# Performance work log

Hardware: AMD Instinct MI355X
Metric: run time of the kernel (lower is better)

Reference implementation:

```python
import jax, jax.numpy as jnp
import numpy as np

NUM_HEADS = 12
HEAD_DIM = 64
SCALE = HEAD_DIM ** -0.5


def setup_inputs() -> dict:
    key = jax.random.key(0)
    ks = jax.random.split(key, 5)
    B, N, C = 8, 1024, 768
    x = jax.random.normal(ks[0], (B, N, C), dtype=jnp.float32)
    qkv_w = jax.random.normal(ks[1], (3 * C, C), dtype=jnp.float32) * (C ** -0.5)
    qkv_b = jax.random.normal(ks[2], (3 * C,), dtype=jnp.float32) * 0.02
    proj_w = jax.random.normal(ks[3], (C, C), dtype=jnp.float32) * (C ** -0.5)
    proj_b = jax.random.normal(ks[4], (C,), dtype=jnp.float32) * 0.02
    return {"x": x, "qkv_w": qkv_w, "qkv_b": qkv_b, "proj_w": proj_w, "proj_b": proj_b}


def reference(x, qkv_w, qkv_b, proj_w, proj_b):
    B, N, C = x.shape
    H, D = NUM_HEADS, HEAD_DIM
    # qkv projection: (B,N,3C) -> (3,B,H,N,D)
    qkv = (x @ qkv_w.T + qkv_b).reshape(B, N, 3, H, D).transpose(2, 0, 3, 1, 4)
    q, k, v = qkv[0], qkv[1], qkv[2]
    q = q * SCALE
    # full N x N attention scores, softmax over keys
    attn = jax.nn.softmax(jnp.einsum("bhnd,bhmd->bhnm", q, k), axis=-1)
    # Libragrad: detach the softmax map before multiplying with V
    attn = jax.lax.stop_gradient(attn)
    out = jnp.einsum("bhnm,bhmd->bhnd", attn, v)  # (B,H,N,D)
    out = out.transpose(0, 2, 1, 3).reshape(B, N, C)
    return out @ proj_w.T + proj_b
```

## Files before the change

kernel.cpp:

```cpp
#include <hip/hip_runtime.h>

#define NH 12
#define HD 64
#define BB 8
#define SEQ 1024
#define CD 768

typedef __bf16 bf16x8 __attribute__((ext_vector_type(8)));
typedef float f32x4 __attribute__((ext_vector_type(4)));

__device__ __forceinline__ unsigned short f2bf(float f) {
    unsigned int u = __float_as_uint(f);
    u = (u + 0x7fffu + ((u >> 16) & 1u)) >> 16;
    return (unsigned short)u;
}

__device__ __forceinline__ void gld_lds16(const unsigned short* g, unsigned short* l) {
    __builtin_amdgcn_global_load_lds(
        (const __attribute__((address_space(1))) unsigned int*)g,
        (__attribute__((address_space(3))) unsigned int*)l, 16, 0, 0);
}

#define N4_X 1572864
#define N4_W1 442368
#define N4_W2 147456
__global__ void cast_all(const float* __restrict__ x, const float* __restrict__ w1,
                         const float* __restrict__ w2,
                         unsigned short* __restrict__ ox, unsigned short* __restrict__ ow1,
                         unsigned short* __restrict__ ow2) {
    int i = blockIdx.x * blockDim.x + threadIdx.x;
    const float4* src;
    ushort4* dst;
    if (i < N4_X) {
        src = (const float4*)x + i; dst = (ushort4*)ox + i;
    } else if (i < N4_X + N4_W1) {
        src = (const float4*)w1 + (i - N4_X); dst = (ushort4*)ow1 + (i - N4_X);
    } else if (i < N4_X + N4_W1 + N4_W2) {
        src = (const float4*)w2 + (i - N4_X - N4_W1); dst = (ushort4*)ow2 + (i - N4_X - N4_W1);
    } else return;
    float4 f = *src;
    ushort4 o;
    o.x = f2bf(f.x); o.y = f2bf(f.y); o.z = f2bf(f.z); o.w = f2bf(f.w);
    *dst = o;
}

template<int MODE>
__global__ __launch_bounds__(256)
void gemm_bt(const unsigned short* __restrict__ A, const unsigned short* __restrict__ W,
             const float* __restrict__ bias,
             unsigned short* __restrict__ qb, unsigned short* __restrict__ kb,
             unsigned short* __restrict__ vb, float* __restrict__ fout,
             int M, int N, int K) {
    __shared__ __attribute__((aligned(16))) unsigned short As[128 * 32];
    __shared__ __attribute__((aligned(16))) unsigned short Bs[128 * 32];

    const int t    = threadIdx.x;
    const int bm0  = blockIdx.x * 128;
    const int bn0  = blockIdx.y * 128;
    const int wave = t >> 6;
    const int lane = t & 63;
    const int wm   = (wave >> 1) * 64;
    const int wn   = (wave & 1) * 64;
    const int col  = lane & 15;
    const int quad = lane >> 4;

    const int srow = t >> 2;
    const int scol = (t & 3) * 8;

    f32x4 acc[4][4];
#pragma unroll
    for (int i = 0; i < 4; i++)
#pragma unroll
        for (int j = 0; j < 4; j++) acc[i][j] = (f32x4){0.f, 0.f, 0.f, 0.f};

    for (int k0 = 0; k0 < K; k0 += 32) {
        __syncthreads();
        gld_lds16(A + (size_t)(bm0 + srow) * K + k0 + scol,      As + srow * 32 + scol);
        gld_lds16(A + (size_t)(bm0 + 64 + srow) * K + k0 + scol, As + (64 + srow) * 32 + scol);
        gld_lds16(W + (size_t)(bn0 + srow) * K + k0 + scol,      Bs + srow * 32 + scol);
        gld_lds16(W + (size_t)(bn0 + 64 + srow) * K + k0 + scol, Bs + (64 + srow) * 32 + scol);
        __syncthreads();

        bf16x8 af[4], bf[4];
#pragma unroll
        for (int mi = 0; mi < 4; mi++)
            af[mi] = *(const bf16x8*)(As + (wm + mi * 16 + col) * 32 + quad * 8);
#pragma unroll
        for (int ni = 0; ni < 4; ni++)
            bf[ni] = *(const bf16x8*)(Bs + (wn + ni * 16 + col) * 32 + quad * 8);
#pragma unroll
        for (int mi = 0; mi < 4; mi++)
#pragma unroll
            for (int ni = 0; ni < 4; ni++)
                acc[mi][ni] = __builtin_amdgcn_mfma_f32_16x16x32_bf16(
                    af[mi], bf[ni], acc[mi][ni], 0, 0, 0);
    }

    if (MODE == 1) {
#pragma unroll
        for (int mi = 0; mi < 4; mi++)
#pragma unroll
            for (int ni = 0; ni < 4; ni++) {
                const int n = bn0 + wn + ni * 16 + col;
                const float bv = bias[n];
#pragma unroll
                for (int r = 0; r < 4; r++) {
                    const int m = bm0 + wm + mi * 16 + quad * 4 + r;
                    fout[(size_t)m * N + n] = acc[mi][ni][r] + bv;
                }
            }
        return;
    }

    const int sel = bn0 / 768;
    const int nb  = bn0 - sel * 768;
    const int b   = bm0 >> 10;
    const int nqb = bm0 & 1023;

    if (sel == 2) {
#pragma unroll
        for (int ni = 0; ni < 4; ni++) {
            const int hn = nb + wn + ni * 16;
            const int h  = hn >> 6;
            const int d0 = hn & 63;
            const float bv = bias[bn0 + wn + ni * 16 + col];
            unsigned short* const rowb =
                vb + ((size_t)(b * NH + h) * HD + d0 + col) * SEQ + nqb + wm;
#pragma unroll
            for (int mi = 0; mi < 4; mi++) {
                ushort4 o;
                o.x = f2bf(acc[mi][ni][0] + bv);
                o.y = f2bf(acc[mi][ni][1] + bv);
                o.z = f2bf(acc[mi][ni][2] + bv);
                o.w = f2bf(acc[mi][ni][3] + bv);
                *(ushort4*)(rowb + mi * 16 + quad * 4) = o;
            }
        }
        return;
    }

    unsigned short* const dstbuf = (sel == 0) ? qb : kb;
    const float scale = (sel == 0) ? 0.18033688f : 1.0f;

#pragma unroll
    for (int ni = 0; ni < 4; ni++) {
        const int hn = nb + wn + ni * 16;
        const int h  = hn >> 6;
        const int d0 = hn & 63;
        const float bv = bias[bn0 + wn + ni * 16 + col];
        unsigned short* const rowbase =
            dstbuf + ((size_t)(b * NH + h) * SEQ) * HD + d0 + col;
#pragma unroll
        for (int mi = 0; mi < 4; mi++)
#pragma unroll
            for (int r = 0; r < 4; r++) {
                const int nq = nqb + wm + mi * 16 + quad * 4 + r;
                rowbase[(size_t)nq * HD] = f2bf((acc[mi][ni][r] + bv) * scale);
            }
    }
}

__global__ __launch_bounds__(256, 3)
void attn_mfma(const unsigned short* __restrict__ qb,
               const unsigned short* __restrict__ kb,
               const unsigned short* __restrict__ vb,
               unsigned short* __restrict__ ob) {
    __shared__ __attribute__((aligned(16))) unsigned short Ks[64 * 72];
    __shared__ __attribute__((aligned(16))) unsigned short VT[64 * 72];
    __shared__ __attribute__((aligned(16))) unsigned short Ps[128 * 76];

    const int t  = threadIdx.x;
    const int bh = blockIdx.x;
    const int qt = blockIdx.y;
    const size_t base = (size_t)bh * SEQ * HD;

    const int sr = t >> 2;
    const int sc = (t & 3) * 16;

    const int wave = t >> 6;
    const int lane = t & 63;
    const int col  = lane & 15;
    const int quad = lane >> 4;

    bf16x8 aq[2][2];
#pragma unroll
    for (int u = 0; u < 2; u++) {
        const int q = qt * 128 + (2 * wave + u) * 16 + col;
        aq[u][0] = *(const bf16x8*)(qb + base + (size_t)q * HD + quad * 8);
        aq[u][1] = *(const bf16x8*)(qb + base + (size_t)q * HD + 32 + quad * 8);
    }

    float l_r[2] = {0.f, 0.f};
    f32x4 accO[2][4];
#pragma unroll
    for (int u = 0; u < 2; u++)
#pragma unroll
        for (int di = 0; di < 4; di++) accO[u][di] = (f32x4){0.f, 0.f, 0.f, 0.f};

    const unsigned short* kp = kb + base + (size_t)sr * HD + sc;
    const unsigned short* vp = vb + base + (size_t)sr * SEQ + sc;
    uint4 kr0 = *(const uint4*)kp,  kr1 = *(const uint4*)(kp + 8);
    uint4 vr0 = *(const uint4*)vp,  vr1 = *(const uint4*)(vp + 8);

    for (int kc = 0; kc < 16; kc++) {
        __syncthreads();
        *(uint4*)(Ks + sr * 72 + sc)     = kr0;
        *(uint4*)(Ks + sr * 72 + sc + 8) = kr1;
        *(uint4*)(VT + sr * 72 + sc)     = vr0;
        *(uint4*)(VT + sr * 72 + sc + 8) = vr1;
        __syncthreads();

        if (kc < 15) {
            const unsigned short* kn = kp + (size_t)(kc + 1) * 64 * HD;
            const unsigned short* vn = vp + (size_t)(kc + 1) * 64;
            kr0 = *(const uint4*)kn; kr1 = *(const uint4*)(kn + 8);
            vr0 = *(const uint4*)vn; vr1 = *(const uint4*)(vn + 8);
        }

        f32x4 accT[2][4];
#pragma unroll
        for (int ni = 0; ni < 4; ni++) {
            bf16x8 bk0 = *(const bf16x8*)(Ks + (ni * 16 + col) * 72 + quad * 8);
            bf16x8 bk1 = *(const bf16x8*)(Ks + (ni * 16 + col) * 72 + 32 + quad * 8);
#pragma unroll
            for (int u = 0; u < 2; u++) {
                f32x4 z = (f32x4){0.f, 0.f, 0.f, 0.f};
                z = __builtin_amdgcn_mfma_f32_16x16x32_bf16(bk0, aq[u][0], z, 0, 0, 0);
                z = __builtin_amdgcn_mfma_f32_16x16x32_bf16(bk1, aq[u][1], z, 0, 0, 0);
                accT[u][ni] = z;
            }
        }

#pragma unroll
        for (int u = 0; u < 2; u++) {
            const int prow = (2 * wave + u) * 16;
#pragma unroll
            for (int ni = 0; ni < 4; ni++) {
                float p0 = __builtin_exp2f(accT[u][ni][0]);
                float p1 = __builtin_exp2f(accT[u][ni][1]);
                float p2 = __builtin_exp2f(accT[u][ni][2]);
                float p3 = __builtin_exp2f(accT[u][ni][3]);
                l_r[u] += (p0 + p1) + (p2 + p3);
                union { __bf16 b[4]; uint2 u2; } pk;
                pk.b[0] = (__bf16)p0; pk.b[1] = (__bf16)p1;
                pk.b[2] = (__bf16)p2; pk.b[3] = (__bf16)p3;
                *(uint2*)(Ps + (prow + col) * 76 + ni * 16 + quad * 4) = pk.u2;
            }
        }

        bf16x8 ap[2][2];
#pragma unroll
        for (int u = 0; u < 2; u++) {
            const int prow = (2 * wave + u) * 16;
            ap[u][0] = *(const bf16x8*)(Ps + (prow + col) * 76 + quad * 8);
            ap[u][1] = *(const bf16x8*)(Ps + (prow + col) * 76 + 32 + quad * 8);
        }
#pragma unroll
        for (int di = 0; di < 4; di++) {
            bf16x8 bv0 = *(const bf16x8*)(VT + (di * 16 + col) * 72 + quad * 8);
            bf16x8 bv1 = *(const bf16x8*)(VT + (di * 16 + col) * 72 + 32 + quad * 8);
#pragma unroll
            for (int u = 0; u < 2; u++) {
                accO[u][di] = __builtin_amdgcn_mfma_f32_16x16x32_bf16(ap[u][0], bv0, accO[u][di], 0, 0, 0);
                accO[u][di] = __builtin_amdgcn_mfma_f32_16x16x32_bf16(ap[u][1], bv1, accO[u][di], 0, 0, 0);
            }
        }
    }

    const int b = bh / NH, h = bh - b * NH;
#pragma unroll
    for (int u = 0; u < 2; u++) {
        float s = l_r[u];
        s += __shfl_xor(s, 16);
        s += __shfl_xor(s, 32);
#pragma unroll
        for (int r = 0; r < 4; r++) {
            const float inv = 1.f / __shfl(s, quad * 4 + r);
            const int q = qt * 128 + (2 * wave + u) * 16 + quad * 4 + r;
            const size_t rowbase = ((size_t)b * SEQ + q) * CD + h * 64;
#pragma unroll
            for (int di = 0; di < 4; di++)
                ob[rowbase + di * 16 + col] = f2bf(accO[u][di][r] * inv);
        }
    }
}

extern "C" void kernel_launch(void* const* d_in, const int* in_sizes, int n_in,
                              void* d_out, int out_size, void* d_ws, size_t ws_size,
                              hipStream_t stream) {
    const float* x      = (const float*)d_in[0];
    const float* qkv_w  = (const float*)d_in[1];
    const float* qkv_b  = (const float*)d_in[2];
    const float* proj_w = (const float*)d_in[3];
    const float* proj_b = (const float*)d_in[4];
    float* out = (float*)d_out;

    char* ws = (char*)d_ws;
    unsigned short* x_bf     = (unsigned short*)ws;
    unsigned short* attn_bf  = x_bf;
    unsigned short* qkvw_bf  = (unsigned short*)(ws + 12582912);
    unsigned short* projw_bf = (unsigned short*)(ws + 12582912 + 3538944);
    unsigned short* q_bf     = (unsigned short*)(ws + 12582912 + 3538944 + 1179648);
    unsigned short* k_bf     = q_bf + 6291456;
    unsigned short* v_bf     = k_bf + 6291456;

    cast_all<<<8448, 256, 0, stream>>>(x, qkv_w, proj_w, x_bf, qkvw_bf, projw_bf);

    gemm_bt<0><<<dim3(64, 18), 256, 0, stream>>>(x_bf, qkvw_bf, qkv_b,
                                                 q_bf, k_bf, v_bf, nullptr,
                                                 8192, 2304, 768);

    attn_mfma<<<dim3(96, 8), 256, 0, stream>>>(q_bf, k_bf, v_bf, attn_bf);

    gemm_bt<1><<<dim3(64, 6), 256, 0, stream>>>(attn_bf, projw_bf, proj_b,
                                                nullptr, nullptr, nullptr, out,
                                                8192, 768, 768);
}
```

Before: 212.8 us.

## Double GEMM K-tile to 64 and move V transpose into a separate kernel

The GEMM K tile grows from 32 to 64, so each block barrier pair now covers twice the MFMA work and the k-loop runs half as many iterations. The QKV epilogue now writes V in the same row-major layout as Q and K, replacing the strided transposed ushort4 stores. A new vtrans kernel then transposes V through LDS into the layout attention expects. The cost is an extra launch and one more read and write of V, plus double the LDS for the GEMM tiles.

```diff
diff --git a/kernel.cpp b/kernel.cpp
--- a/kernel.cpp
+++ b/kernel.cpp
@@ -51,8 +51,8 @@
              unsigned short* __restrict__ qb, unsigned short* __restrict__ kb,
              unsigned short* __restrict__ vb, float* __restrict__ fout,
              int M, int N, int K) {
-    __shared__ __attribute__((aligned(16))) unsigned short As[128 * 32];
-    __shared__ __attribute__((aligned(16))) unsigned short Bs[128 * 32];
+    __shared__ __attribute__((aligned(16))) unsigned short As[128 * 64];
+    __shared__ __attribute__((aligned(16))) unsigned short Bs[128 * 64];
 
     const int t    = threadIdx.x;
     const int bm0  = blockIdx.x * 128;
@@ -64,8 +64,8 @@
     const int col  = lane & 15;
     const int quad = lane >> 4;
 
-    const int srow = t >> 2;
-    const int scol = (t & 3) * 8;
+    const int srow = t >> 3;
+    const int scol = (t & 7) * 8;
 
     f32x4 acc[4][4];
 #pragma unroll
@@ -73,27 +73,37 @@
 #pragma unroll
         for (int j = 0; j < 4; j++) acc[i][j] = (f32x4){0.f, 0.f, 0.f, 0.f};
 
-    for (int k0 = 0; k0 < K; k0 += 32) {
+    for (int k0 = 0; k0 < K; k0 += 64) {
         __syncthreads();
-        gld_lds16(A + (size_t)(bm0 + srow) * K + k0 + scol,      As + srow * 32 + scol);
-        gld_lds16(A + (size_t)(bm0 + 64 + srow) * K + k0 + scol, As + (64 + srow) * 32 + scol);
-        gld_lds16(W + (size_t)(bn0 + srow) * K + k0 + scol,      Bs + srow * 32 + scol);
-        gld_lds16(W + (size_t)(bn0 + 64 + srow) * K + k0 + scol, Bs + (64 + srow) * 32 + scol);
+#pragma unroll
+        for (int p = 0; p < 4; p++) {
+            gld_lds16(A + (size_t)(bm0 + p * 32 + srow) * K + k0 + scol,
+                      As + (p * 32 + srow) * 64 + scol);
+            gld_lds16(W + (size_t)(bn0 + p * 32 + srow) * K + k0 + scol,
+                      Bs + (p * 32 + srow) * 64 + scol);
+        }
         __syncthreads();
 
-        bf16x8 af[4], bf[4];
+        bf16x8 af[4][2], bf[4][2];
 #pragma unroll
         for (int mi = 0; mi < 4; mi++)
-            af[mi] = *(const bf16x8*)(As + (wm + mi * 16 + col) * 32 + quad * 8);
+#pragma unroll
+            for (int h = 0; h < 2; h++)
+                af[mi][h] = *(const bf16x8*)(As + (wm + mi * 16 + col) * 64 + h * 32 + quad * 8);
 #pragma unroll
         for (int ni = 0; ni < 4; ni++)
-            bf[ni] = *(const bf16x8*)(Bs + (wn + ni * 16 + col) * 32 + quad * 8);
+#pragma unroll
+            for (int h = 0; h < 2; h++)
+                bf[ni][h] = *(const bf16x8*)(Bs + (wn + ni * 16 + col) * 64 + h * 32 + quad * 8);
 #pragma unroll
         for (int mi = 0; mi < 4; mi++)
 #pragma unroll
-            for (int ni = 0; ni < 4; ni++)
+            for (int ni = 0; ni < 4; ni++) {
                 acc[mi][ni] = __builtin_amdgcn_mfma_f32_16x16x32_bf16(
-                    af[mi], bf[ni], acc[mi][ni], 0, 0, 0);
+                    af[mi][0], bf[ni][0], acc[mi][ni], 0, 0, 0);
+                acc[mi][ni] = __builtin_amdgcn_mfma_f32_16x16x32_bf16(
+                    af[mi][1], bf[ni][1], acc[mi][ni], 0, 0, 0);
+            }
     }
 
     if (MODE == 1) {
@@ -116,30 +126,7 @@
     const int nb  = bn0 - sel * 768;
     const int b   = bm0 >> 10;
     const int nqb = bm0 & 1023;
-
-    if (sel == 2) {
-#pragma unroll
-        for (int ni = 0; ni < 4; ni++) {
-            const int hn = nb + wn + ni * 16;
-            const int h  = hn >> 6;
-            const int d0 = hn & 63;
-            const float bv = bias[bn0 + wn + ni * 16 + col];
-            unsigned short* const rowb =
-                vb + ((size_t)(b * NH + h) * HD + d0 + col) * SEQ + nqb + wm;
-#pragma unroll
-            for (int mi = 0; mi < 4; mi++) {
-                ushort4 o;
-                o.x = f2bf(acc[mi][ni][0] + bv);
-                o.y = f2bf(acc[mi][ni][1] + bv);
-                o.z = f2bf(acc[mi][ni][2] + bv);
-                o.w = f2bf(acc[mi][ni][3] + bv);
-                *(ushort4*)(rowb + mi * 16 + quad * 4) = o;
-            }
-        }
-        return;
-    }
-
-    unsigned short* const dstbuf = (sel == 0) ? qb : kb;
+    unsigned short* const dstbuf = (sel == 0) ? qb : (sel == 1) ? kb : vb;
     const float scale = (sel == 0) ? 0.18033688f : 1.0f;
 
 #pragma unroll
@@ -158,6 +145,28 @@
                 rowbase[(size_t)nq * HD] = f2bf((acc[mi][ni][r] + bv) * scale);
             }
     }
+}
+
+__global__ __launch_bounds__(256)
+void vtrans(const unsigned short* __restrict__ v, unsigned short* __restrict__ vt) {
+    __shared__ __attribute__((aligned(16))) unsigned short T[64 * 72];
+    const int bh = blockIdx.x;
+    const int kt = blockIdx.y;
+    const int t  = threadIdx.x;
+    const int r  = t >> 2;
+    const int c  = (t & 3) * 16;
+
+    const unsigned short* src = v + ((size_t)bh * SEQ + kt * 64 + r) * HD + c;
+    *(uint4*)(T + r * 72 + c)     = *(const uint4*)src;
+    *(uint4*)(T + r * 72 + c + 8) = *(const uint4*)(src + 8);
+    __syncthreads();
+
+    union { unsigned short us[16]; uint4 u4[2]; } o;
+#pragma unroll
+    for (int j = 0; j < 16; j++) o.us[j] = T[(c + j) * 72 + r];
+    unsigned short* dst = vt + ((size_t)bh * HD + r) * SEQ + kt * 64 + c;
+    *(uint4*)dst       = o.u4[0];
+    *(uint4*)(dst + 8) = o.u4[1];
 }
 
 __global__ __launch_bounds__(256, 3)
@@ -297,12 +306,13 @@
 
     char* ws = (char*)d_ws;
     unsigned short* x_bf     = (unsigned short*)ws;
-    unsigned short* attn_bf  = x_bf;
     unsigned short* qkvw_bf  = (unsigned short*)(ws + 12582912);
     unsigned short* projw_bf = (unsigned short*)(ws + 12582912 + 3538944);
     unsigned short* q_bf     = (unsigned short*)(ws + 12582912 + 3538944 + 1179648);
     unsigned short* k_bf     = q_bf + 6291456;
     unsigned short* v_bf     = k_bf + 6291456;
+    unsigned short* vt_bf    = x_bf;
+    unsigned short* attn_bf  = v_bf;
 
     cast_all<<<8448, 256, 0, stream>>>(x, qkv_w, proj_w, x_bf, qkvw_bf, projw_bf);
 
@@ -310,7 +320,9 @@
                                                  q_bf, k_bf, v_bf, nullptr,
                                                  8192, 2304, 768);
 
-    attn_mfma<<<dim3(96, 8), 256, 0, stream>>>(q_bf, k_bf, v_bf, attn_bf);
+    vtrans<<<dim3(96, 16), 256, 0, stream>>>(v_bf, vt_bf);
+
+    attn_mfma<<<dim3(96, 8), 256, 0, stream>>>(q_bf, k_bf, vt_bf, attn_bf);
 
     gemm_bt<1><<<dim3(64, 6), 256, 0, stream>>>(attn_bf, projw_bf, proj_b,
                                                 nullptr, nullptr, nullptr, out,
```

New measurement: 214.9 us. No clear change (+1.0%).
